# Kernel optimization log

Hardware: AMD Instinct MI355X
Metric: run time of the kernel (lower is better)

## Reference

```python
import jax, jax.numpy as jnp
import numpy as np

STRIDE = (1, 1)
PAD = 1


def _conv2d(x, w):
    # NCHW conv, OIHW kernel, stride 1, padding 1 (module defaults)
    return jax.lax.conv_general_dilated(
        x, w, window_strides=STRIDE, padding=[(PAD, PAD), (PAD, PAD)],
        dimension_numbers=("NCHW", "OIHW", "NCHW"))


def setup_inputs() -> dict:
    key = jax.random.key(0)
    k1, k2, k3 = jax.random.split(key, 3)
    C, H, W, O, KH, KW = 16, 16, 16, 32, 3, 3
    N = C * H * W  # 4096 flat input features
    base = jax.random.normal(k1, (1, N), dtype=jnp.float32)
    return {
        "x": base,
        "lower_bound": base - 0.1,
        "upper_bound": base + 0.1,
        "input_shape": jnp.array([1, C, H, W], dtype=jnp.int32),
        "kernel": 0.1 * jax.random.normal(k2, (O, C, KH, KW), dtype=jnp.float32),
        "bias": 0.1 * jax.random.normal(k3, (O,), dtype=jnp.float32),
    }


def reference(x, lower_bound, upper_bound, input_shape, kernel, bias):
    shape = tuple(int(s) for s in np.asarray(input_shape))  # (1, C, H, W)
    x4 = x.reshape(shape)
    lb4 = lower_bound.reshape(shape)
    ub4 = upper_bound.reshape(shape)

    # twice inside F.conv2d and once via the explicit reshape-add)
    neg_w = jnp.where(kernel < 0, kernel, 0.0)
    pos_w = jnp.where(kernel >= 0, kernel, 0.0)
    b3 = (3.0 * bias)[None, :, None, None]
    lb_new = _conv2d(ub4, neg_w) + _conv2d(lb4, pos_w) + b3
    ub_new = _conv2d(lb4, neg_w) + _conv2d(ub4, pos_w) + b3
    lb_new = lb_new.reshape(lb_new.shape[0], -1)
    ub_new = ub_new.reshape(ub_new.shape[0], -1)

    # concrete forward through the conv layer (bias once)
    x_out4 = _conv2d(x4, kernel) + bias[None, :, None, None]
    x_out = x_out4.reshape(x_out4.shape[0], -1)

    # unroll conv into an explicit [numel_in, numel_out] matrix.
    # Equivalent to the source's eye().view + conv3d(depth-1 kernel):
    # each basis image is convolved independently -> batched conv2d.
    N = x.shape[1]
    eye_imgs = jnp.eye(N, dtype=kernel.dtype).reshape((N,) + shape[1:])  # [N,C,H,W]
    unrolled = _conv2d(eye_imgs, kernel)  # [N, O, H', W']
    weights = unrolled.reshape(N, -1)     # [numel_in, O*H'*W']
    O_, Hp, Wp = unrolled.shape[1:]
    bias_vec = jnp.broadcast_to(bias[:, None, None], (O_, Hp, Wp)).reshape(-1)

    return (x_out, lb_new, ub_new, weights, bias_vec)
```

## Files before the change

### kernel.cpp

```cpp
#include <hip/hip_runtime.h>

#define O_CH  32
#define C_CH  16
#define HH    16
#define WW    16
#define NPIX  256
#define NIN   4096
#define NOUT  8192

__global__ void conv_bounds_kernel(const float* __restrict__ x,
                                   const float* __restrict__ lb,
                                   const float* __restrict__ ub,
                                   const float* __restrict__ wk,
                                   const float* __restrict__ bias,
                                   float* __restrict__ out) {
    int t = blockIdx.x * blockDim.x + threadIdx.x;
    if (t >= NOUT) return;
    int o  = t >> 8;
    int ph = (t >> 4) & 15;
    int pw = t & 15;
    float xa = 0.f, la = 0.f, ua = 0.f;
    #pragma unroll
    for (int c = 0; c < C_CH; ++c) {
        const float* kb = wk + (o * C_CH + c) * 9;
        #pragma unroll
        for (int kh = 0; kh < 3; ++kh) {
            int h = ph + kh - 1;
            if ((unsigned)h >= (unsigned)HH) continue;
            #pragma unroll
            for (int kw = 0; kw < 3; ++kw) {
                int w = pw + kw - 1;
                if ((unsigned)w >= (unsigned)WW) continue;
                float k = kb[kh * 3 + kw];
                int idx = c * NPIX + h * WW + w;
                float xv = x[idx];
                float lv = lb[idx];
                float uv = ub[idx];
                xa = fmaf(k, xv, xa);
                if (k < 0.f) {
                    la = fmaf(k, uv, la);
                    ua = fmaf(k, lv, ua);
                } else {
                    la = fmaf(k, lv, la);
                    ua = fmaf(k, uv, ua);
                }
            }
        }
    }
    float b = bias[o];
    out[t]            = xa + b;
    out[NOUT + t]     = la + 3.f * b;
    out[2 * NOUT + t] = ua + 3.f * b;
}

__global__ void weights_kernel(const float* __restrict__ wk,
                               const float* __restrict__ bias,
                               float* __restrict__ weights,
                               float* __restrict__ bias_vec) {
    const int total4 = NIN * (NOUT / 4);
    int stride = gridDim.x * blockDim.x;
    for (int i = blockIdx.x * blockDim.x + threadIdx.x; i < total4; i += stride) {
        int n  = i >> 11;
        int r  = i & 2047;
        int o  = r >> 6;
        int p  = r & 63;
        int ph = p >> 2;
        int pw0 = (p & 3) << 2;
        int c = n >> 8;
        int h = (n >> 4) & 15;
        int w = n & 15;
        float4 v = make_float4(0.f, 0.f, 0.f, 0.f);
        int kh = h - ph + 1;
        if ((unsigned)kh < 3u) {
            const float* kb = wk + ((o * C_CH + c) * 3 + kh) * 3;
            int kw0 = w - pw0 + 1;
            if ((unsigned)(kw0)     < 3u) v.x = kb[kw0];
            if ((unsigned)(kw0 - 1) < 3u) v.y = kb[kw0 - 1];
            if ((unsigned)(kw0 - 2) < 3u) v.z = kb[kw0 - 2];
            if ((unsigned)(kw0 - 3) < 3u) v.w = kb[kw0 - 3];
        }
        reinterpret_cast<float4*>(weights)[i] = v;
    }
    int t = blockIdx.x * blockDim.x + threadIdx.x;
    if (t < NOUT) bias_vec[t] = bias[t >> 8];
}

extern "C" void kernel_launch(void* const* d_in, const int* in_sizes, int n_in,
                              void* d_out, int out_size, void* d_ws, size_t ws_size,
                              hipStream_t stream) {
    const float* x    = (const float*)d_in[0];
    const float* lbp  = (const float*)d_in[1];
    const float* ubp  = (const float*)d_in[2];
    const float* wk   = (const float*)d_in[4];
    const float* bias = (const float*)d_in[5];

    float* out = (float*)d_out;
    float* x_out    = out;
    float* weights  = out + 3 * NOUT;
    float* bias_vec = out + 3 * NOUT + (size_t)NIN * NOUT;

    conv_bounds_kernel<<<NOUT / 256, 256, 0, stream>>>(x, lbp, ubp, wk, bias, x_out);

    weights_kernel<<<2048, 256, 0, stream>>>(wk, bias, weights, bias_vec);
}
```

Baseline: 167.1 us.

## Fuse bounds conv and unrolled-weights kernels into one launch with streaming stores

Merges the interval-bound convolution and the unrolled weight-matrix generation into a single kernel, with the first 32 blocks doing the bounds and the rest writing the weight matrix. The bounds path stages inputs and kernel weights in shared memory. The weights path gives each block one input row set and 16 consecutive width positions, so the shifted kernel taps are reused across rows, and it writes them with nontemporal stores. This removes one launch and reduces index math on the 128MB write-bound output. The large shared-memory allocation applies to every block, including the weight blocks that never use it, which may limit occupancy for the dominant write path.

```diff
diff --git a/kernel.cpp b/kernel.cpp
--- a/kernel.cpp
+++ b/kernel.cpp
@@ -7,82 +7,102 @@
 #define NPIX  256
 #define NIN   4096
 #define NOUT  8192
+#define NB_BOUNDS  32
+#define NB_WEIGHTS 2048
 
-__global__ void conv_bounds_kernel(const float* __restrict__ x,
-                                   const float* __restrict__ lb,
-                                   const float* __restrict__ ub,
-                                   const float* __restrict__ wk,
-                                   const float* __restrict__ bias,
-                                   float* __restrict__ out) {
-    int t = blockIdx.x * blockDim.x + threadIdx.x;
-    if (t >= NOUT) return;
-    int o  = t >> 8;
-    int ph = (t >> 4) & 15;
-    int pw = t & 15;
-    float xa = 0.f, la = 0.f, ua = 0.f;
-    #pragma unroll
-    for (int c = 0; c < C_CH; ++c) {
-        const float* kb = wk + (o * C_CH + c) * 9;
+typedef float v4f __attribute__((ext_vector_type(4)));
+
+
+__global__ __launch_bounds__(256) void fused_deeppoly_kernel(
+    const float* __restrict__ x,
+    const float* __restrict__ lb,
+    const float* __restrict__ ub,
+    const float* __restrict__ wk,
+    const float* __restrict__ bias,
+    float* __restrict__ out) {
+    __shared__ float sx[NIN], sl[NIN], su[NIN], skw[C_CH * 9];
+    const int b   = blockIdx.x;
+    const int tid = threadIdx.x;
+
+    if (b < NB_BOUNDS) {
+        const v4f* x4 = (const v4f*)x;
+        const v4f* l4 = (const v4f*)lb;
+        const v4f* u4 = (const v4f*)ub;
+        v4f* sx4 = (v4f*)sx; v4f* sl4 = (v4f*)sl; v4f* su4 = (v4f*)su;
         #pragma unroll
-        for (int kh = 0; kh < 3; ++kh) {
-            int h = ph + kh - 1;
-            if ((unsigned)h >= (unsigned)HH) continue;
+        for (int k = 0; k < 4; ++k) {
+            int i = tid + k * 256;
+            sx4[i] = x4[i]; sl4[i] = l4[i]; su4[i] = u4[i];
+        }
+        const int o = b;
+        if (tid < C_CH * 9) skw[tid] = wk[o * C_CH * 9 + tid];
+        __syncthreads();
+
+        const int ph = tid >> 4, pw = tid & 15;
+        float xa = 0.f, la = 0.f, ua = 0.f;
+        #pragma unroll
+        for (int c = 0; c < C_CH; ++c) {
             #pragma unroll
-            for (int kw = 0; kw < 3; ++kw) {
-                int w = pw + kw - 1;
-                if ((unsigned)w >= (unsigned)WW) continue;
-                float k = kb[kh * 3 + kw];
-                int idx = c * NPIX + h * WW + w;
-                float xv = x[idx];
-                float lv = lb[idx];
-                float uv = ub[idx];
-                xa = fmaf(k, xv, xa);
-                if (k < 0.f) {
-                    la = fmaf(k, uv, la);
-                    ua = fmaf(k, lv, ua);
-                } else {
-                    la = fmaf(k, lv, la);
-                    ua = fmaf(k, uv, ua);
+            for (int kh = 0; kh < 3; ++kh) {
+                int h = ph + kh - 1;
+                if ((unsigned)h >= (unsigned)HH) continue;
+                #pragma unroll
+                for (int kw = 0; kw < 3; ++kw) {
+                    int w = pw + kw - 1;
+                    if ((unsigned)w >= (unsigned)WW) continue;
+                    float k   = skw[c * 9 + kh * 3 + kw];
+                    int   idx = c * NPIX + h * WW + w;
+                    xa = fmaf(k, sx[idx], xa);
+                    float lv = sl[idx], uv = su[idx];
+                    la = fmaf(k, (k < 0.f) ? uv : lv, la);
+                    ua = fmaf(k, (k < 0.f) ? lv : uv, ua);
                 }
             }
         }
-    }
-    float b = bias[o];
-    out[t]            = xa + b;
-    out[NOUT + t]     = la + 3.f * b;
-    out[2 * NOUT + t] = ua + 3.f * b;
-}
+        const int   t  = o * 256 + tid;
+        const float bv = bias[o];
+        out[t]            = xa + bv;
+        out[NOUT + t]     = la + 3.f * bv;
+        out[2 * NOUT + t] = ua + 3.f * bv;
+        out[(size_t)3 * NOUT + (size_t)NIN * NOUT + t] = bv;
+    } else {
+        const int b2       = b - NB_BOUNDS;
+        const int colgroup = b2 & 7;
+        const int rowset   = b2 >> 3;
+        const int r   = colgroup * 256 + tid;
+        const int o   = r >> 6;
+        const int p   = r & 63;
+        const int ph  = p >> 2;
+        const int pw0 = (p & 3) << 2;
+        const int c   = rowset >> 4;
+        const int h   = rowset & 15;
+        const int kh  = h - ph + 1;
 
-__global__ void weights_kernel(const float* __restrict__ wk,
-                               const float* __restrict__ bias,
-                               float* __restrict__ weights,
-                               float* __restrict__ bias_vec) {
-    const int total4 = NIN * (NOUT / 4);
-    int stride = gridDim.x * blockDim.x;
-    for (int i = blockIdx.x * blockDim.x + threadIdx.x; i < total4; i += stride) {
-        int n  = i >> 11;
-        int r  = i & 2047;
-        int o  = r >> 6;
-        int p  = r & 63;
-        int ph = p >> 2;
-        int pw0 = (p & 3) << 2;
-        int c = n >> 8;
-        int h = (n >> 4) & 15;
-        int w = n & 15;
-        float4 v = make_float4(0.f, 0.f, 0.f, 0.f);
-        int kh = h - ph + 1;
+        float k0 = 0.f, k1 = 0.f, k2 = 0.f;
         if ((unsigned)kh < 3u) {
             const float* kb = wk + ((o * C_CH + c) * 3 + kh) * 3;
-            int kw0 = w - pw0 + 1;
-            if ((unsigned)(kw0)     < 3u) v.x = kb[kw0];
-            if ((unsigned)(kw0 - 1) < 3u) v.y = kb[kw0 - 1];
-            if ((unsigned)(kw0 - 2) < 3u) v.z = kb[kw0 - 2];
-            if ((unsigned)(kw0 - 3) < 3u) v.w = kb[kw0 - 3];
+            k0 = kb[0]; k1 = kb[1]; k2 = kb[2];
         }
-        reinterpret_cast<float4*>(weights)[i] = v;
+        auto sel = [&](int kw) -> float {
+            return kw == 0 ? k0 : (kw == 1 ? k1 : (kw == 2 ? k2 : 0.f));
+        };
+
+        v4f* wout = (v4f*)(out + 3 * NOUT);
+        v4f* pptr = wout + (size_t)(rowset * 16) * 2048 + r;
+
+        v4f v;
+        v.x = sel(1 - pw0);
+        v.y = sel(-pw0);
+        v.z = sel(-1 - pw0);
+        v.w = sel(-2 - pw0);
+        #pragma unroll
+        for (int j = 0; j < 16; ++j) {
+            __builtin_nontemporal_store(v, pptr);
+            pptr += 2048;
+            v.w = v.z; v.z = v.y; v.y = v.x;
+            v.x = sel(j + 2 - pw0);
+        }
     }
-    int t = blockIdx.x * blockDim.x + threadIdx.x;
-    if (t < NOUT) bias_vec[t] = bias[t >> 8];
 }
 
 extern "C" void kernel_launch(void* const* d_in, const int* in_sizes, int n_in,
@@ -94,12 +114,6 @@
     const float* wk   = (const float*)d_in[4];
     const float* bias = (const float*)d_in[5];
 
-    float* out = (float*)d_out;
-    float* x_out    = out;
-    float* weights  = out + 3 * NOUT;
-    float* bias_vec = out + 3 * NOUT + (size_t)NIN * NOUT;
-
-    conv_bounds_kernel<<<NOUT / 256, 256, 0, stream>>>(x, lbp, ubp, wk, bias, x_out);
-
-    weights_kernel<<<2048, 256, 0, stream>>>(wk, bias, weights, bias_vec);
+    fused_deeppoly_kernel<<<NB_BOUNDS + NB_WEIGHTS, 256, 0, stream>>>(
+        x, lbp, ubp, wk, bias, (float*)d_out);
 }
```

Result: faster. 148.4 us (-11.2%).
